# Kernel tuning notes

Hardware: AMD Instinct MI355X
Metric: run time of the kernel (lower is better)

The kernel has to match this reference:

```python
import jax, jax.numpy as jnp
import numpy as np

B, N0, FEAT, NHID, GDIM = 32, 2048, 1036, 128, 32
DEG = 16
E = B * N0 * DEG
K1, K2, K3 = 410, 82, 17  # ceil(0.2*{2048,410,82}) per SAGPooling stage


def _segsum(v, idx, n):
    return jax.ops.segment_sum(v, idx, num_segments=n)


def sage_conv(x, src, dst, em, Wl, bl, Wr, n):
    # PyG SAGEConv: lin_l(mean_{j->i} x_j) + lin_r(x_i); lin applied before the
    # (linear) mean -> identical math, messages are NHID-dim not FEAT-dim.
    h = x @ Wl
    s = _segsum(h[src] * em[:, None], dst, n)
    cnt = _segsum(em, dst, n)
    return s / jnp.maximum(cnt, 1.0)[:, None] + bl + x @ Wr


def gcn_score(x, src, dst, em, W, b, n):
    # 1-channel GCNConv with self-loops and symmetric normalization.
    h = x @ W  # [n, 1]
    deg = 1.0 + _segsum(em, dst, n)  # +1 for self loop
    dis = jax.lax.rsqrt(deg)
    norm = dis[src] * dis[dst] * em
    agg = _segsum(h[src] * norm[:, None], dst, n) + h / deg[:, None]
    return (agg + b)[:, 0]


def sag_pool(x, src, dst, em, W, b, n_per, k):
    # Equal-size graphs -> static top-k per graph; dropped edges masked, not removed.
    nb = x.shape[0] // n_per
    score = gcn_score(x, src, dst, em, W, b, x.shape[0])
    _, idx = jax.lax.top_k(score.reshape(nb, n_per), k)
    perm = (idx + (jnp.arange(nb) * n_per)[:, None]).reshape(-1)
    xn = x[perm] * jnp.tanh(score[perm])[:, None]
    inv = jnp.full((x.shape[0],), -1, jnp.int32).at[perm].set(
        jnp.arange(nb * k, dtype=jnp.int32))
    ns, nd = inv[src], inv[dst]
    emn = em * ((ns >= 0) & (nd >= 0)).astype(em.dtype)
    return xn, jnp.maximum(ns, 0), jnp.maximum(nd, 0), emn


def readout(x, k):
    r = x.reshape(B, k, NHID)
    return jnp.concatenate([r.max(axis=1), r.mean(axis=1)], axis=1)  # [B, 2*NHID]


def graphnet(x, src, dst, W1l, b1l, W1r, Wp1, bp1, W2l, b2l, W2r, Wp2, bp2,
             W3l, b3l, W3r, Wp3, bp3, lin1_w, lin1_b, lin2_w, lin2_b, lin3_w, lin3_b):
    # NormalizeFeaturesV2: first 12 cols / column max
    mx = jnp.max(x[:, :12], axis=0)
    x = jnp.concatenate([x[:, :12] / mx, x[:, 12:]], axis=1)
    em = jnp.ones((E,), x.dtype)

    x = jax.nn.relu(sage_conv(x, src, dst, em, W1l, b1l, W1r, B * N0))
    x, s1, d1, e1 = sag_pool(x, src, dst, em, Wp1, bp1, N0, K1)
    x1 = readout(x, K1)

    x = jax.nn.relu(sage_conv(x, s1, d1, e1, W2l, b2l, W2r, B * K1))
    x, s2, d2, e2 = sag_pool(x, s1, d1, e1, Wp2, bp2, K1, K2)
    x2 = readout(x, K2)

    x = jax.nn.relu(sage_conv(x, s2, d2, e2, W3l, b3l, W3r, B * K2))
    x, s3, d3, e3 = sag_pool(x, s2, d2, e2, Wp3, bp3, K2, K3)
    x3 = readout(x, K3)

    h = x1 + x2 + x3
    h = jax.nn.relu(h @ lin1_w + lin1_b)  # dropout is identity at eval
    features = jax.nn.relu(h @ lin2_w + lin2_b)
    out = features @ lin3_w + lin3_b  # act=None
    return features, out


def setup_inputs():
    key = jax.random.key(0)
    ks = jax.random.split(key, 16)
    x = jax.random.normal(ks[0], (B * N0, FEAT), jnp.float32)
    e = jax.random.randint(ks[1], (2, B, N0 * DEG), 0, N0)
    ei = (e + (jnp.arange(B) * N0)[None, :, None]).reshape(2, -1).astype(jnp.int32)

    def lin(k, fi, fo):
        return (jax.random.normal(k, (fi, fo), jnp.float32) / np.sqrt(fi)).astype(jnp.float32)

    z = lambda *s: jnp.zeros(s, jnp.float32)
    return dict(
        x=x, src=ei[0], dst=ei[1],
        W1l=lin(ks[2], FEAT, NHID), b1l=z(NHID), W1r=lin(ks[3], FEAT, NHID),
        Wp1=lin(ks[4], NHID, 1), bp1=z(1),
        W2l=lin(ks[5], NHID, NHID), b2l=z(NHID), W2r=lin(ks[6], NHID, NHID),
        Wp2=lin(ks[7], NHID, 1), bp2=z(1),
        W3l=lin(ks[8], NHID, NHID), b3l=z(NHID), W3r=lin(ks[9], NHID, NHID),
        Wp3=lin(ks[10], NHID, 1), bp3=z(1),
        lin1_w=lin(ks[11], 2 * NHID, NHID), lin1_b=z(NHID),
        lin2_w=lin(ks[12], NHID, GDIM), lin2_b=z(GDIM),
        lin3_w=lin(ks[13], GDIM, 1), lin3_b=z(1),
    )


def reference(x, src, dst, W1l, b1l, W1r, Wp1, bp1, W2l, b2l, W2r, Wp2, bp2,
              W3l, b3l, W3r, Wp3, bp3, lin1_w, lin1_b, lin2_w, lin2_b, lin3_w, lin3_b):
    return graphnet(x, src, dst, W1l, b1l, W1r, Wp1, bp1, W2l, b2l, W2r, Wp2, bp2,
                    W3l, b3l, W3r, Wp3, bp3, lin1_w, lin1_b, lin2_w, lin2_b,
                    lin3_w, lin3_b)
```

## Files before the change

kernel.cpp:

```cpp
#include <hip/hip_runtime.h>

typedef unsigned int u32;
typedef unsigned short u16;

#define NB 32
#define N0V 2048
#define FEATV 1036
#define EDGESV (NB*N0V*16)
#define KK1 410
#define KK2 82
#define KK3 17
#define NN1 (NB*N0V)
#define NN2 (NB*KK1)
#define NN3 (NB*KK2)
#define NN4 (NB*KK3)
#define KSTEP1 33
#define KSTEP2 4
#define ESTR 32768

typedef __bf16 bf16x8 __attribute__((ext_vector_type(8)));
typedef float f32x4 __attribute__((ext_vector_type(4)));

__device__ inline u16 f2bf(float f){
  u32 u = __float_as_uint(f);
  u32 r = (u + 0x7FFFu + ((u >> 16) & 1u)) >> 16;
  return (u16)r;
}
__device__ inline float bf2f(u16 h){ return __uint_as_float(((u32)h) << 16); }
__device__ inline float dec_ord(u32 u){
  u32 bits = (u & 0x80000000u) ? (u ^ 0x80000000u) : ~u;
  return __uint_as_float(bits);
}
__device__ inline u16 bfbits(__bf16 b){ union{__bf16 f; u16 u;} c; c.f=b; return c.u; }
__device__ inline void cvt4c(float4 v, ushort4& h, ushort4& l){
  __bf16 h0=(__bf16)v.x, h1=(__bf16)v.y, h2=(__bf16)v.z, h3=(__bf16)v.w;
  float r0=v.x-(float)h0, r1=v.y-(float)h1, r2=v.z-(float)h2, r3=v.w-(float)h3;
  h.x=bfbits(h0); h.y=bfbits(h1); h.z=bfbits(h2); h.w=bfbits(h3);
  l.x=bfbits((__bf16)r0); l.y=bfbits((__bf16)r1);
  l.z=bfbits((__bf16)r2); l.w=bfbits((__bf16)r3);
}
__device__ inline void gload_lds16(const void* g, void* l){
  __builtin_amdgcn_global_load_lds(
      (const __attribute__((address_space(1))) unsigned int*)g,
      (__attribute__((address_space(3))) unsigned int*)l, 16, 0, 0);
}

__global__ void init_kernel(u32* mx){
  if (threadIdx.x < 12) mx[threadIdx.x] = 0;
}
__global__ void fill0(int* p, int n){
  int i = blockIdx.x*256 + threadIdx.x;
  if (i < n) p[i] = 0;
}

__global__ void colmax_kernel(const float* __restrict__ x, u32* mx){
  __shared__ float sm[256];
  int t = threadIdx.x;
  int r = blockIdx.x*256 + t;
  const float4* p = (const float4*)(x + (size_t)r*FEATV);
  float4 v0 = p[0], v1 = p[1], v2 = p[2];
  float m[12] = {v0.x,v0.y,v0.z,v0.w, v1.x,v1.y,v1.z,v1.w, v2.x,v2.y,v2.z,v2.w};
  for (int j=0;j<12;j++){
    sm[t] = m[j]; __syncthreads();
    for (int off=128; off>0; off>>=1){ if (t<off) sm[t]=fmaxf(sm[t],sm[t+off]); __syncthreads(); }
    if (t==0){
      u32 b = __float_as_uint(sm[0]);
      u32 u = (b & 0x80000000u) ? ~b : (b | 0x80000000u);
      atomicMax(&mx[j], u);
    }
    __syncthreads();
  }
}

__global__ void wprep_all(const float* __restrict__ W1l, const float* __restrict__ W1r,
                          const float* __restrict__ W2l, const float* __restrict__ W2r,
                          const float* __restrict__ W3l, const float* __restrict__ W3r,
                          const u32* __restrict__ mxo,
                          u16* __restrict__ B1h, u16* __restrict__ B1l,
                          u16* __restrict__ B2h, u16* __restrict__ B2l,
                          u16* __restrict__ B3h, u16* __restrict__ B3l){
  int idx = blockIdx.x*256 + threadIdx.x;
  const float *Wl, *Wr; u16 *oh, *ol; int K, o, scale12;
  if (idx < KSTEP1*8192){ Wl=W1l; Wr=W1r; oh=B1h; ol=B1l; K=FEATV; o=idx; scale12=1; }
  else if (idx < (KSTEP1+KSTEP2)*8192){ Wl=W2l; Wr=W2r; oh=B2h; ol=B2l; K=128; o=idx-KSTEP1*8192; scale12=0; }
  else if (idx < (KSTEP1+2*KSTEP2)*8192){ Wl=W3l; Wr=W3r; oh=B3h; ol=B3l; K=128; o=idx-(KSTEP1+KSTEP2)*8192; scale12=0; }
  else return;
  int kt = o >> 13, r13 = o & 8191;
  int khg = r13 >> 11, n = (r13 >> 3) & 255, kk8 = r13 & 7;
  int k = (kt << 5) + khg*8 + kk8;
  float v = 0.f;
  if (k < K) v = (n < 128) ? Wl[(size_t)k*128 + n] : Wr[(size_t)k*128 + (n-128)];
  if (scale12 && k < 12) v /= dec_ord(mxo[k]);
  u16 h = f2bf(v);
  oh[o] = h;
  ol[o] = f2bf(v - bf2f(h));
}

__global__ void histf(const int* __restrict__ src, const int* __restrict__ dst,
                      const int* __restrict__ inv1, const int* __restrict__ inv2,
                      int np1, int nperOut, int* __restrict__ deg){
  int e = blockIdx.x*256 + threadIdx.x;
  if (e >= EDGESV) return;
  int s = src[e], d = dst[e];
  int g = d >> 11;
  int ls, ld;
  if (inv1){
    ls = inv1[s]; ld = inv1[d];
    if ((ls | ld) < 0) return;
    if (inv2){
      ls = inv2[g*np1 + ls]; ld = inv2[g*np1 + ld];
      if ((ls | ld) < 0) return;
    }
  } else { ld = d & 2047; }
  atomicAdd(&deg[g*nperOut + ld], 1);
}

__launch_bounds__(1024)
__global__ void scank(const int* __restrict__ deg, int nper,
                      int* __restrict__ rps, int* __restrict__ cur){
  __shared__ int part[1024];
  int g = blockIdx.x, t = threadIdx.x;
  int chunk = (nper + 1023) >> 10;
  int c0 = t*chunk, ss = 0;
  for (int u = 0; u < chunk; ++u){ int i = c0+u; if (i < nper) ss += deg[g*nper + i]; }
  part[t] = ss; __syncthreads();
  for (int off = 1; off < 1024; off <<= 1){
    int v = (t >= off) ? part[t-off] : 0;
    __syncthreads();
    part[t] += v;
    __syncthreads();
  }
  int run = part[t] - ss;
  for (int u = 0; u < chunk; ++u){
    int i = c0+u;
    if (i < nper){
      int pos = g*ESTR + run;
      rps[g*nper + i] = pos;
      cur[g*nper + i] = pos;
      run += deg[g*nper + i];
    }
  }
}

__global__ void scatf(const int* __restrict__ src, const int* __restrict__ dst,
                      const int* __restrict__ inv1, const int* __restrict__ inv2,
                      int np1, int nperOut, int* __restrict__ cur, int* __restrict__ adj){
  int e = blockIdx.x*256 + threadIdx.x;
  if (e >= EDGESV) return;
  int s = src[e], d = dst[e];
  int g = d >> 11;
  int ls, ld;
  if (inv1){
    ls = inv1[s]; ld = inv1[d];
    if ((ls | ld) < 0) return;
    if (inv2){
      ls = inv2[g*np1 + ls]; ld = inv2[g*np1 + ld];
      if ((ls | ld) < 0) return;
    }
  } else { ls = s & 2047; ld = d & 2047; }
  int p = atomicAdd(&cur[g*nperOut + ld], 1);
  adj[p] = ls;
}

__launch_bounds__(256, 2)
__global__ void gemm_kernel(const float* __restrict__ A, int lda,
                            int Kvalid, int Ksteps,
                            const u16* __restrict__ Bth, const u16* __restrict__ Btl,
                            float* __restrict__ hl, float* __restrict__ hr){
  __shared__ __align__(16) u16 Ah[2][2048];
  __shared__ __align__(16) u16 Al[2][2048];
  __shared__ __align__(16) u16 Bh[2][8192];
  __shared__ __align__(16) u16 Bl[2][8192];
  int tid = threadIdx.x;
  int row0 = blockIdx.x * 64;
  int w = tid >> 6, lane = tid & 63;
  int lr = lane & 15, kh = lane >> 4;

  int p0i = tid, p1i = tid + 256;
  int kg0 = p0i >> 7, rw0 = (p0i & 127) >> 1, hf0 = p0i & 1;
  int kg1 = p1i >> 7, rw1 = (p1i & 127) >> 1, hf1 = p1i & 1;
  int coff0 = kg0*8 + hf0*4, coff1 = kg1*8 + hf1*4;
  const float* pA0 = A + (size_t)(row0 + rw0)*lda + coff0;
  const float* pA1 = A + (size_t)(row0 + rw1)*lda + coff1;
  int wi0 = kg0*512 + rw0*8 + hf0*4;
  int wi1 = kg1*512 + rw1*8 + hf1*4;

  f32x4 acc[4][4];
  #pragma unroll
  for (int i=0;i<4;i++)
    #pragma unroll
    for (int j=0;j<4;j++) acc[i][j] = (f32x4){0.f,0.f,0.f,0.f};

  float4 z4 = make_float4(0.f,0.f,0.f,0.f);

#define LOADA(KT, V0, V1) { int k0_ = (KT)<<5; \
    V0 = (k0_ + coff0 < Kvalid) ? *(const float4*)(pA0 + k0_) : z4; \
    V1 = (k0_ + coff1 < Kvalid) ? *(const float4*)(pA1 + k0_) : z4; }

#define ISSUEB(KT, BUF) { size_t tb_ = (size_t)(KT)*8192; \
    _Pragma("unroll") \
    for (int j_=0;j_<4;j_++){ int o_ = j_*2048 + w*512; \
      gload_lds16(Bth + tb_ + o_ + lane*8, &Bh[BUF][o_]); \
      gload_lds16(Btl + tb_ + o_ + lane*8, &Bl[BUF][o_]); } }

#define CVTWRITE(V0, V1, BUF) { ushort4 h_, l_; \
    cvt4c(V0, h_, l_); *(ushort4*)&Ah[BUF][wi0] = h_; *(ushort4*)&Al[BUF][wi0] = l_; \
    cvt4c(V1, h_, l_); *(ushort4*)&Ah[BUF][wi1] = h_; *(ushort4*)&Al[BUF][wi1] = l_; }

  float4 a0, a1, pp0, pp1;
  LOADA(0, a0, a1);
  ISSUEB(0, 0);
  LOADA(1, pp0, pp1);
  CVTWRITE(a0, a1, 0);
  asm volatile("s_waitcnt lgkmcnt(0)" ::: "memory");
  asm volatile("s_waitcnt vmcnt(2)" ::: "memory");
  __builtin_amdgcn_s_barrier();

  for (int kt = 0; kt < Ksteps; ++kt){
    int cur = kt & 1, nxt = cur ^ 1;
    if (kt+1 < Ksteps) ISSUEB(kt+1, nxt);
    float4 n0 = z4, n1 = z4;
    if (kt+2 < Ksteps) LOADA(kt+2, n0, n1);
    if (kt+2 < Ksteps)      asm volatile("s_waitcnt vmcnt(12)" ::: "memory");
    else if (kt+1 < Ksteps) asm volatile("s_waitcnt vmcnt(10)" ::: "memory");
    else                    asm volatile("s_waitcnt vmcnt(0)"  ::: "memory");

    bf16x8 fah[4], fal[4], fbh[4], fbl[4];
    #pragma unroll
    for (int mi=0;mi<4;mi++){
      int idx = kh*512 + (mi*16 + lr)*8;
      fah[mi] = *(const bf16x8*)&Ah[cur][idx];
      fal[mi] = *(const bf16x8*)&Al[cur][idx];
    }
    #pragma unroll
    for (int ni=0;ni<4;ni++){
      int idx = kh*2048 + (w*64 + ni*16 + lr)*8;
      fbh[ni] = *(const bf16x8*)&Bh[cur][idx];
      fbl[ni] = *(const bf16x8*)&Bl[cur][idx];
    }
    if (kt+1 < Ksteps) CVTWRITE(pp0, pp1, nxt);
    asm volatile("s_waitcnt lgkmcnt(0)" ::: "memory");
    __builtin_amdgcn_sched_barrier(0);
    __builtin_amdgcn_s_setprio(1);
    #pragma unroll
    for (int mi=0;mi<4;mi++)
      #pragma unroll
      for (int ni=0;ni<4;ni++){
        acc[mi][ni] = __builtin_amdgcn_mfma_f32_16x16x32_bf16(fah[mi], fbh[ni], acc[mi][ni], 0,0,0);
        acc[mi][ni] = __builtin_amdgcn_mfma_f32_16x16x32_bf16(fah[mi], fbl[ni], acc[mi][ni], 0,0,0);
        acc[mi][ni] = __builtin_amdgcn_mfma_f32_16x16x32_bf16(fal[mi], fbh[ni], acc[mi][ni], 0,0,0);
      }
    __builtin_amdgcn_s_setprio(0);
    pp0 = n0; pp1 = n1;
    __builtin_amdgcn_s_barrier();
  }
#undef LOADA
#undef ISSUEB
#undef CVTWRITE
  float* dst = (w < 2) ? hl : hr;
  #pragma unroll
  for (int mi=0;mi<4;mi++)
    #pragma unroll
    for (int j=0;j<4;j++){
      int row = row0 + mi*16 + kh*4 + j;
      #pragma unroll
      for (int ni=0;ni<4;ni++){
        int ch = (w*64 + ni*16 + lr) & 127;
        dst[(size_t)row*128 + ch] = acc[mi][ni][j];
      }
    }
}

__global__ void convfin_w(const float* __restrict__ hl, const float* __restrict__ hr,
                          const int* __restrict__ rps,
                          const int* __restrict__ rpd, const int* __restrict__ adj,
                          const float* __restrict__ bl, const float* __restrict__ Wp,
                          float* __restrict__ xout, float* __restrict__ hsc,
                          int nper, int bpg, int xcdMap){
  int b = blockIdx.x, t = threadIdx.x;
  int g, slot;
  if (xcdMap){ int xcd = b & 7, idx = b >> 3; g = xcd + 8*(idx >> 8); slot = idx & 255; }
  else { g = b / bpg; slot = b - g*bpg; }
  int wv = t >> 6, lane = t & 63;
  int sub = lane >> 5, l32 = lane & 31;
  int i = slot*8 + wv*2 + sub;
  if (i >= nper) return;
  int gbase = g*nper;
  int gi = gbase + i;
  int s = rps[gi], d = rpd[gi];
  const int* ap = adj + s;
  float4 a = make_float4(0.f,0.f,0.f,0.f);
  int e = 0;
  for (; e + 8 <= d; e += 8){
    int j0=ap[e],j1=ap[e+1],j2=ap[e+2],j3=ap[e+3];
    int j4=ap[e+4],j5=ap[e+5],j6=ap[e+6],j7=ap[e+7];
    float4 v0 = *(const float4*)(hl + (size_t)(gbase+j0)*128 + l32*4);
    float4 v1 = *(const float4*)(hl + (size_t)(gbase+j1)*128 + l32*4);
    float4 v2 = *(const float4*)(hl + (size_t)(gbase+j2)*128 + l32*4);
    float4 v3 = *(const float4*)(hl + (size_t)(gbase+j3)*128 + l32*4);
    float4 v4 = *(const float4*)(hl + (size_t)(gbase+j4)*128 + l32*4);
    float4 v5 = *(const float4*)(hl + (size_t)(gbase+j5)*128 + l32*4);
    float4 v6 = *(const float4*)(hl + (size_t)(gbase+j6)*128 + l32*4);
    float4 v7 = *(const float4*)(hl + (size_t)(gbase+j7)*128 + l32*4);
    a.x += v0.x+v1.x+v2.x+v3.x+v4.x+v5.x+v6.x+v7.x;
    a.y += v0.y+v1.y+v2.y+v3.y+v4.y+v5.y+v6.y+v7.y;
    a.z += v0.z+v1.z+v2.z+v3.z+v4.z+v5.z+v6.z+v7.z;
    a.w += v0.w+v1.w+v2.w+v3.w+v4.w+v5.w+v6.w+v7.w;
  }
  for (; e < d; ++e){
    float4 hj = *(const float4*)(hl + (size_t)(gbase + ap[e])*128 + l32*4);
    a.x += hj.x; a.y += hj.y; a.z += hj.z; a.w += hj.w;
  }
  float invc = 1.0f / fmaxf((float)d, 1.0f);
  float4 hrv = *(const float4*)(hr + (size_t)gi*128 + l32*4);
  float4 bb = *(const float4*)(bl + l32*4);
  float4 o;
  o.x = fmaxf(a.x*invc + bb.x + hrv.x, 0.f);
  o.y = fmaxf(a.y*invc + bb.y + hrv.y, 0.f);
  o.z = fmaxf(a.z*invc + bb.z + hrv.z, 0.f);
  o.w = fmaxf(a.w*invc + bb.w + hrv.w, 0.f);
  *(float4*)(xout + (size_t)gi*128 + l32*4) = o;
  float4 wp = *(const float4*)(Wp + l32*4);
  float v = o.x*wp.x + o.y*wp.y + o.z*wp.z + o.w*wp.w;
  #pragma unroll
  for (int m = 16; m > 0; m >>= 1) v += __shfl_xor(v, m);
  if (l32 == 0) hsc[gi] = v;
}

__global__ void scoreagg_w(const float* __restrict__ hsc, const int* __restrict__ rps,
                           const int* __restrict__ rpd, const int* __restrict__ adj,
                           const float* __restrict__ bp, int nper,
                           u32* __restrict__ su){
  int g = blockIdx.y;
  int i = blockIdx.x*256 + threadIdx.x;
  if (i >= nper) return;
  int gbase = g*nper;
  int gi = gbase + i;
  float di = 1.0f + (float)rpd[gi];
  float a = hsc[gi] / di;
  float rdi = rsqrtf(di);
  int s = rps[gi], d = rpd[gi];
  #pragma unroll 4
  for (int e = s; e < s+d; ++e){
    int j = gbase + adj[e];
    a += hsc[j] * rsqrtf(1.0f + (float)rpd[j]) * rdi;
  }
  float sc = a + bp[0];
  u32 b = __float_as_uint(sc);
  su[gi] = (b & 0x80000000u) ? ~b : (b | 0x80000000u);
}

__launch_bounds__(512)
__global__ void topkpool(const u32* __restrict__ suG, const float* __restrict__ xin,
                         int nper, int k,
                         float* __restrict__ xp, float* __restrict__ r,
                         int* __restrict__ invG){
  __shared__ u32 su[2048];
  __shared__ int bins[256], sfx[256];
  __shared__ int slist[416];
  __shared__ int tlist[64];
  __shared__ float smx[512], ssm[512];
  __shared__ u32 spfx;
  __shared__ int srem, ssel, stie;
  int g = blockIdx.x, t = threadIdx.x;
  int gbase = g*nper;
  for (int i = t; i < nper; i += 512){
    su[i] = suG[gbase + i];
    invG[gbase + i] = -1;
  }
  if (t == 0){ spfx = 0; srem = k; ssel = 0; stie = 0; }
  __syncthreads();
  for (int pass = 0; pass < 4; ++pass){
    int shift = 24 - 8*pass;
    if (t < 256) bins[t] = 0;
    __syncthreads();
    u32 pfx = spfx; int rem = srem;
    for (int i = t; i < nper; i += 512){
      u32 u = su[i];
      if (pass == 0 || (u >> (shift+8)) == (pfx >> (shift+8)))
        atomicAdd(&bins[(u >> shift) & 255], 1);
    }
    __syncthreads();
    if (t < 256) sfx[t] = bins[t];
    __syncthreads();
    for (int off=1; off<256; off<<=1){
      int v = 0;
      if (t < 256 && t + off < 256) v = sfx[t+off];
      __syncthreads();
      if (t < 256) sfx[t] += v;
      __syncthreads();
    }
    if (t < 256){
      int above = (t == 255) ? 0 : sfx[t+1];
      if (sfx[t] >= rem && above < rem){
        spfx = pfx | ((u32)t << shift);
        srem = rem - above;
      }
    }
    __syncthreads();
  }
  u32 th = spfx;
  for (int i = t; i < nper; i += 512)
    if (su[i] > th){ int p = atomicAdd(&ssel, 1); slist[p] = i; }
  __syncthreads();
  for (int i = t; i < nper; i += 512)
    if (su[i] == th){ int q = atomicAdd(&stie, 1); if (q < 64) tlist[q] = i; }
  __syncthreads();
  if (t == 0){
    int p = ssel, need = k - p;
    if (need > 0){
      if (stie <= 64){
        for (int a = 1; a < stie; ++a){
          int v = tlist[a], b2 = a-1;
          while (b2 >= 0 && tlist[b2] > v){ tlist[b2+1] = tlist[b2]; b2--; }
          tlist[b2+1] = v;
        }
        for (int m = 0; m < need; ++m) slist[p+m] = tlist[m];
      } else {
        for (int i = 0; i < nper && p < k; ++i)
          if (su[i] == th) slist[p++] = i;
      }
    }
  }
  __syncthreads();
  int q = t >> 7, c = t & 127;
  float mxv = -3.4e38f, smv = 0.f;
  for (int j = q; j < k; j += 4){
    int li = slist[j];
    float ts = tanhf(dec_ord(su[li]));
    float vv = xin[((size_t)(gbase + li))*128 + c] * ts;
    xp[((size_t)(g*k + j))*128 + c] = vv;
    mxv = fmaxf(mxv, vv); smv += vv;
  }
  smx[t] = mxv; ssm[t] = smv;
  for (int j = t; j < k; j += 512) invG[gbase + slist[j]] = j;
  __syncthreads();
  if (t < 128){
    r[g*256 + t] = fmaxf(fmaxf(smx[t], smx[t+128]), fmaxf(smx[t+256], smx[t+384]));
    r[g*256 + 128 + t] = (ssm[t]+ssm[t+128]+ssm[t+256]+ssm[t+384]) / (float)k;
  }
}

__global__ void head_kernel(const float* __restrict__ r1, const float* __restrict__ r2,
                            const float* __restrict__ r3,
                            const float* __restrict__ w1, const float* __restrict__ b1,
                            const float* __restrict__ w2, const float* __restrict__ b2,
                            const float* __restrict__ w3, const float* __restrict__ b3,
                            float* __restrict__ out){
  __shared__ float hs[32][256];
  __shared__ float h1[32][128];
  __shared__ float ft[32][32];
  int t = threadIdx.x;
  for (int o = t; o < 32*256; o += 256) hs[o>>8][o&255] = r1[o]+r2[o]+r3[o];
  __syncthreads();
  for (int o = t; o < 32*128; o += 256){
    int i = o >> 7, j = o & 127;
    float a = b1[j];
    for (int c = 0; c < 256; ++c) a += hs[i][c]*w1[c*128 + j];
    h1[i][j] = fmaxf(a, 0.f);
  }
  __syncthreads();
  for (int o = t; o < 32*32; o += 256){
    int i = o >> 5, j = o & 31;
    float a = b2[j];
    for (int c = 0; c < 128; ++c) a += h1[i][c]*w2[c*32 + j];
    float v = fmaxf(a, 0.f);
    ft[i][j] = v;
    out[o] = v;
  }
  __syncthreads();
  if (t < 32){
    float a = b3[0];
    for (int c = 0; c < 32; ++c) a += ft[t][c]*w3[c];
    out[1024 + t] = a;
  }
}

extern "C" void kernel_launch(void* const* d_in, const int* in_sizes, int n_in,
                              void* d_out, int out_size, void* d_ws, size_t ws_size,
                              hipStream_t stream){
  (void)in_sizes; (void)n_in; (void)out_size; (void)ws_size;
  const float* x   = (const float*)d_in[0];
  const int* esrc  = (const int*)d_in[1];
  const int* edst  = (const int*)d_in[2];
  const float* W1l = (const float*)d_in[3];
  const float* b1l = (const float*)d_in[4];
  const float* W1r = (const float*)d_in[5];
  const float* Wp1 = (const float*)d_in[6];
  const float* bp1 = (const float*)d_in[7];
  const float* W2l = (const float*)d_in[8];
  const float* b2l = (const float*)d_in[9];
  const float* W2r = (const float*)d_in[10];
  const float* Wp2 = (const float*)d_in[11];
  const float* bp2 = (const float*)d_in[12];
  const float* W3l = (const float*)d_in[13];
  const float* b3l = (const float*)d_in[14];
  const float* W3r = (const float*)d_in[15];
  const float* Wp3 = (const float*)d_in[16];
  const float* bp3 = (const float*)d_in[17];
  const float* l1w = (const float*)d_in[18];
  const float* l1b = (const float*)d_in[19];
  const float* l2w = (const float*)d_in[20];
  const float* l2b = (const float*)d_in[21];
  const float* l3w = (const float*)d_in[22];
  const float* l3b = (const float*)d_in[23];
  float* out = (float*)d_out;

  char* ws = (char*)d_ws;
  size_t off = 0;
  auto alloc = [&](size_t bytes)->char*{
    char* p = ws + off; off = (off + bytes + 255) & ~(size_t)255; return p;
  };

  u32* mx    = (u32*)alloc(64);
  size_t z0 = off;
  int* deg1  = (int*)alloc((size_t)NN1*4);
  int* deg2  = (int*)alloc((size_t)NN2*4);
  int* deg3  = (int*)alloc((size_t)NN3*4);
  size_t zend = off;
  int* rps   = (int*)alloc((size_t)NN1*4);
  int* curB  = (int*)alloc((size_t)NN1*4);
  int* adj   = (int*)alloc((size_t)EDGESV*4);
  u16* B1h   = (u16*)alloc((size_t)KSTEP1*8192*2);
  u16* B1l   = (u16*)alloc((size_t)KSTEP1*8192*2);
  u16* B2h   = (u16*)alloc((size_t)KSTEP2*8192*2);
  u16* B2l   = (u16*)alloc((size_t)KSTEP2*8192*2);
  u16* B3h   = (u16*)alloc((size_t)KSTEP2*8192*2);
  u16* B3l   = (u16*)alloc((size_t)KSTEP2*8192*2);
  float* hlb = (float*)alloc((size_t)NN1*128*4);
  float* hrb = (float*)alloc((size_t)NN1*128*4);
  float* x1    = (float*)alloc((size_t)NN1*128*4);
  float* x2    = (float*)alloc((size_t)NN2*128*4);
  float* x3    = (float*)alloc((size_t)NN3*128*4);
  float* xp1   = (float*)alloc((size_t)NN2*128*4);
  float* xp2   = (float*)alloc((size_t)NN3*128*4);
  float* xp3   = (float*)alloc((size_t)NN4*128*4);
  float* hsc   = (float*)alloc((size_t)NN1*4);
  u32* suG     = (u32*)alloc((size_t)NN1*4);
  int* inv1G   = (int*)alloc((size_t)NN1*4);
  int* inv2G   = (int*)alloc((size_t)NN2*4);
  int* inv3G   = (int*)alloc((size_t)NN3*4);
  float* r1    = (float*)alloc((size_t)32*256*4);
  float* r2    = (float*)alloc((size_t)32*256*4);
  float* r3    = (float*)alloc((size_t)32*256*4);

  int zn = (int)((zend - z0) / 4);
  init_kernel<<<1, 64, 0, stream>>>(mx);
  fill0<<<(zn+255)/256, 256, 0, stream>>>((int*)(ws+z0), zn);
  colmax_kernel<<<256, 256, 0, stream>>>(x, mx);
  wprep_all<<<((KSTEP1+2*KSTEP2)*8192+255)/256, 256, 0, stream>>>(
      W1l, W1r, W2l, W2r, W3l, W3r, mx, B1h, B1l, B2h, B2l, B3h, B3l);

  histf<<<EDGESV/256, 256, 0, stream>>>(esrc, edst, nullptr, nullptr, 0, N0V, deg1);
  scank<<<NB, 1024, 0, stream>>>(deg1, N0V, rps, curB);
  scatf<<<EDGESV/256, 256, 0, stream>>>(esrc, edst, nullptr, nullptr, 0, N0V, curB, adj);
  gemm_kernel<<<NN1/64, 256, 0, stream>>>(x, FEATV, FEATV, KSTEP1, B1h, B1l, hlb, hrb);
  convfin_w<<<NN1/8, 256, 0, stream>>>(hlb, hrb, rps, deg1, adj, b1l, Wp1, x1, hsc, N0V, 256, 1);
  scoreagg_w<<<dim3(N0V/256, NB), 256, 0, stream>>>(hsc, rps, deg1, adj, bp1, N0V, suG);
  topkpool<<<NB, 512, 0, stream>>>(suG, x1, N0V, KK1, xp1, r1, inv1G);

  histf<<<EDGESV/256, 256, 0, stream>>>(esrc, edst, inv1G, nullptr, 0, KK1, deg2);
  scank<<<NB, 1024, 0, stream>>>(deg2, KK1, rps, curB);
  scatf<<<EDGESV/256, 256, 0, stream>>>(esrc, edst, inv1G, nullptr, 0, KK1, curB, adj);
  gemm_kernel<<<NN2/64, 256, 0, stream>>>(xp1, 128, 128, KSTEP2, B2h, B2l, hlb, hrb);
  convfin_w<<<NB*52, 256, 0, stream>>>(hlb, hrb, rps, deg2, adj, b2l, Wp2, x2, hsc, KK1, 52, 0);
  scoreagg_w<<<dim3((KK1+255)/256, NB), 256, 0, stream>>>(hsc, rps, deg2, adj, bp2, KK1, suG);
  topkpool<<<NB, 512, 0, stream>>>(suG, x2, KK1, KK2, xp2, r2, inv2G);

  histf<<<EDGESV/256, 256, 0, stream>>>(esrc, edst, inv1G, inv2G, KK1, KK2, deg3);
  scank<<<NB, 1024, 0, stream>>>(deg3, KK2, rps, curB);
  scatf<<<EDGESV/256, 256, 0, stream>>>(esrc, edst, inv1G, inv2G, KK1, KK2, curB, adj);
  gemm_kernel<<<NN3/64, 256, 0, stream>>>(xp2, 128, 128, KSTEP2, B3h, B3l, hlb, hrb);
  convfin_w<<<NB*11, 256, 0, stream>>>(hlb, hrb, rps, deg3, adj, b3l, Wp3, x3, hsc, KK2, 11, 0);
  scoreagg_w<<<dim3(1, NB), 256, 0, stream>>>(hsc, rps, deg3, adj, bp3, KK2, suG);
  topkpool<<<NB, 512, 0, stream>>>(suG, x3, KK2, KK3, xp3, r3, inv3G);

  head_kernel<<<1, 256, 0, stream>>>(r1, r2, r3, l1w, l1b, l2w, l2b, l3w, l3b, out);
}
```

Measured before the change: 527.0 us.

## Split stage-1 SAGE aggregation into two channel-half passes plus separate score GEMV

The first-stage neighbor-mean aggregation now runs as two kernels, each gathering only 64 of the 128 channels, with an XCD-aware block mapping. The GCN score projection moves into its own GEMV kernel that reads back x1. The intent is to shrink each pass's gathered working set so neighbor rows stay resident in cache. In exchange, the adjacency lists are read twice, x1 is re-read, and two extra launches are added.

```diff
diff --git a/kernel.cpp b/kernel.cpp
--- a/kernel.cpp
+++ b/kernel.cpp
@@ -271,16 +271,76 @@
     }
 }
 
+__global__ void convfin_half(const float* __restrict__ hl, const float* __restrict__ hr,
+                             const int* __restrict__ rps, const int* __restrict__ rpd,
+                             const int* __restrict__ adj, const float* __restrict__ bl,
+                             float* __restrict__ xout, int c0){
+  int b = blockIdx.x, t = threadIdx.x;
+  int xcd = b & 7, idx = b >> 3;
+  int g = xcd + 8*(idx >> 7);
+  int slot = idx & 127;
+  int wv = t >> 6, lane = t & 63;
+  int sub = lane >> 4, l16 = lane & 15;
+  int i = slot*16 + wv*4 + sub;
+  int gbase = g*N0V;
+  int gi = gbase + i;
+  int s = rps[gi], d = rpd[gi];
+  const int* ap = adj + s;
+  float4 a = make_float4(0.f,0.f,0.f,0.f);
+  int e = 0;
+  for (; e + 8 <= d; e += 8){
+    int j0=ap[e],j1=ap[e+1],j2=ap[e+2],j3=ap[e+3];
+    int j4=ap[e+4],j5=ap[e+5],j6=ap[e+6],j7=ap[e+7];
+    float4 v0 = *(const float4*)(hl + (size_t)(gbase+j0)*128 + c0 + l16*4);
+    float4 v1 = *(const float4*)(hl + (size_t)(gbase+j1)*128 + c0 + l16*4);
+    float4 v2 = *(const float4*)(hl + (size_t)(gbase+j2)*128 + c0 + l16*4);
+    float4 v3 = *(const float4*)(hl + (size_t)(gbase+j3)*128 + c0 + l16*4);
+    float4 v4 = *(const float4*)(hl + (size_t)(gbase+j4)*128 + c0 + l16*4);
+    float4 v5 = *(const float4*)(hl + (size_t)(gbase+j5)*128 + c0 + l16*4);
+    float4 v6 = *(const float4*)(hl + (size_t)(gbase+j6)*128 + c0 + l16*4);
+    float4 v7 = *(const float4*)(hl + (size_t)(gbase+j7)*128 + c0 + l16*4);
+    a.x += v0.x+v1.x+v2.x+v3.x+v4.x+v5.x+v6.x+v7.x;
+    a.y += v0.y+v1.y+v2.y+v3.y+v4.y+v5.y+v6.y+v7.y;
+    a.z += v0.z+v1.z+v2.z+v3.z+v4.z+v5.z+v6.z+v7.z;
+    a.w += v0.w+v1.w+v2.w+v3.w+v4.w+v5.w+v6.w+v7.w;
+  }
+  for (; e < d; ++e){
+    float4 hj = *(const float4*)(hl + (size_t)(gbase + ap[e])*128 + c0 + l16*4);
+    a.x += hj.x; a.y += hj.y; a.z += hj.z; a.w += hj.w;
+  }
+  float invc = 1.0f / fmaxf((float)d, 1.0f);
+  float4 hrv = *(const float4*)(hr + (size_t)gi*128 + c0 + l16*4);
+  float4 bb = *(const float4*)(bl + c0 + l16*4);
+  float4 o;
+  o.x = fmaxf(a.x*invc + bb.x + hrv.x, 0.f);
+  o.y = fmaxf(a.y*invc + bb.y + hrv.y, 0.f);
+  o.z = fmaxf(a.z*invc + bb.z + hrv.z, 0.f);
+  o.w = fmaxf(a.w*invc + bb.w + hrv.w, 0.f);
+  *(float4*)(xout + (size_t)gi*128 + c0 + l16*4) = o;
+}
+
+__global__ void hscgemv(const float* __restrict__ x1, const float* __restrict__ Wp,
+                        float* __restrict__ hsc){
+  int idx = blockIdx.x*256 + threadIdx.x;
+  int wv = idx >> 6, lane = idx & 63;
+  int sub = lane >> 5, l32 = lane & 31;
+  int node = wv*2 + sub;
+  float4 xv = *(const float4*)(x1 + (size_t)node*128 + l32*4);
+  float4 wp = *(const float4*)(Wp + l32*4);
+  float v = xv.x*wp.x + xv.y*wp.y + xv.z*wp.z + xv.w*wp.w;
+  #pragma unroll
+  for (int m = 16; m > 0; m >>= 1) v += __shfl_xor(v, m);
+  if (l32 == 0) hsc[node] = v;
+}
+
 __global__ void convfin_w(const float* __restrict__ hl, const float* __restrict__ hr,
                           const int* __restrict__ rps,
                           const int* __restrict__ rpd, const int* __restrict__ adj,
                           const float* __restrict__ bl, const float* __restrict__ Wp,
                           float* __restrict__ xout, float* __restrict__ hsc,
-                          int nper, int bpg, int xcdMap){
+                          int nper, int bpg){
   int b = blockIdx.x, t = threadIdx.x;
-  int g, slot;
-  if (xcdMap){ int xcd = b & 7, idx = b >> 3; g = xcd + 8*(idx >> 8); slot = idx & 255; }
-  else { g = b / bpg; slot = b - g*bpg; }
+  int g = b / bpg, slot = b - g*bpg;
   int wv = t >> 6, lane = t & 63;
   int sub = lane >> 5, l32 = lane & 31;
   int i = slot*8 + wv*2 + sub;
@@ -555,7 +615,9 @@
   scank<<<NB, 1024, 0, stream>>>(deg1, N0V, rps, curB);
   scatf<<<EDGESV/256, 256, 0, stream>>>(esrc, edst, nullptr, nullptr, 0, N0V, curB, adj);
   gemm_kernel<<<NN1/64, 256, 0, stream>>>(x, FEATV, FEATV, KSTEP1, B1h, B1l, hlb, hrb);
-  convfin_w<<<NN1/8, 256, 0, stream>>>(hlb, hrb, rps, deg1, adj, b1l, Wp1, x1, hsc, N0V, 256, 1);
+  convfin_half<<<NN1/16, 256, 0, stream>>>(hlb, hrb, rps, deg1, adj, b1l, x1, 0);
+  convfin_half<<<NN1/16, 256, 0, stream>>>(hlb, hrb, rps, deg1, adj, b1l, x1, 64);
+  hscgemv<<<NN1/8, 256, 0, stream>>>(x1, Wp1, hsc);
   scoreagg_w<<<dim3(N0V/256, NB), 256, 0, stream>>>(hsc, rps, deg1, adj, bp1, N0V, suG);
   topkpool<<<NB, 512, 0, stream>>>(suG, x1, N0V, KK1, xp1, r1, inv1G);
 
@@ -563,7 +625,7 @@
   scank<<<NB, 1024, 0, stream>>>(deg2, KK1, rps, curB);
   scatf<<<EDGESV/256, 256, 0, stream>>>(esrc, edst, inv1G, nullptr, 0, KK1, curB, adj);
   gemm_kernel<<<NN2/64, 256, 0, stream>>>(xp1, 128, 128, KSTEP2, B2h, B2l, hlb, hrb);
-  convfin_w<<<NB*52, 256, 0, stream>>>(hlb, hrb, rps, deg2, adj, b2l, Wp2, x2, hsc, KK1, 52, 0);
+  convfin_w<<<NB*52, 256, 0, stream>>>(hlb, hrb, rps, deg2, adj, b2l, Wp2, x2, hsc, KK1, 52);
   scoreagg_w<<<dim3((KK1+255)/256, NB), 256, 0, stream>>>(hsc, rps, deg2, adj, bp2, KK1, suG);
   topkpool<<<NB, 512, 0, stream>>>(suG, x2, KK1, KK2, xp2, r2, inv2G);
 
@@ -571,7 +633,7 @@
   scank<<<NB, 1024, 0, stream>>>(deg3, KK2, rps, curB);
   scatf<<<EDGESV/256, 256, 0, stream>>>(esrc, edst, inv1G, inv2G, KK1, KK2, curB, adj);
   gemm_kernel<<<NN3/64, 256, 0, stream>>>(xp2, 128, 128, KSTEP2, B3h, B3l, hlb, hrb);
-  convfin_w<<<NB*11, 256, 0, stream>>>(hlb, hrb, rps, deg3, adj, b3l, Wp3, x3, hsc, KK2, 11, 0);
+  convfin_w<<<NB*11, 256, 0, stream>>>(hlb, hrb, rps, deg3, adj, b3l, Wp3, x3, hsc, KK2, 11);
   scoreagg_w<<<dim3(1, NB), 256, 0, stream>>>(hsc, rps, deg3, adj, bp3, KK2, suG);
   topkpool<<<NB, 512, 0, stream>>>(suG, x3, KK2, KK3, xp3, r3, inv3G);
 
```

Result: slower. 537.7 us (+2.0%).
